# Performance work log

Hardware: AMD Instinct MI355X
Metric: run time of the kernel (lower is better)

Reference implementation:

```python
import jax, jax.numpy as jnp
import numpy as np

D = 256
H = 8
HD = D // H
K = 10
CAP = 500000
B = 256


def setup_inputs() -> dict:
    key = jax.random.key(0)
    ks = jax.random.split(key, 5)
    return {
        "content": jax.random.normal(ks[0], (B, D), dtype=jnp.float32),
        "hologram": jax.random.normal(ks[1], (CAP, D), dtype=jnp.float32),
        "memory_strengths": jnp.ones((CAP,), dtype=jnp.float32),
        "in_proj_w": jax.random.normal(ks[2], (3 * D, D), dtype=jnp.float32) * (1.0 / np.sqrt(D)),
        "in_proj_b": jnp.zeros((3 * D,), dtype=jnp.float32),
        "out_proj_w": jax.random.normal(ks[3], (D, D), dtype=jnp.float32) * (1.0 / np.sqrt(D)),
        "out_proj_b": jnp.zeros((D,), dtype=jnp.float32),
    }


def reference(content, hologram, memory_strengths, in_proj_w, in_proj_b, out_proj_w, out_proj_b):
    # similarities [B, CAP], weighted by per-slot memory strength
    sims = jnp.matmul(content, hologram.T) * memory_strengths[None, :]
    # top-k memory slots per query
    top_vals, top_idx = jax.lax.top_k(sims, K)            # [B, K]
    mem = hologram[top_idx]                               # gather -> [B, K, D]

    # nn.MultiheadAttention (batch_first): packed in-proj split into q/k/v
    wq, wk, wv = in_proj_w[:D], in_proj_w[D:2 * D], in_proj_w[2 * D:]
    bq, bk, bv = in_proj_b[:D], in_proj_b[D:2 * D], in_proj_b[2 * D:]

    q = content @ wq.T + bq                               # [B, D]  (query len 1)
    k = mem @ wk.T + bk                                   # [B, K, D]
    v = mem @ wv.T + bv                                   # [B, K, D]

    qh = q.reshape(B, H, HD)                              # [B, H, HD]
    kh = k.reshape(B, K, H, HD).transpose(0, 2, 1, 3)     # [B, H, K, HD]
    vh = v.reshape(B, K, H, HD).transpose(0, 2, 1, 3)     # [B, H, K, HD]

    scores = jnp.einsum("bhd,bhkd->bhk", qh, kh) / np.sqrt(HD)
    attn = jax.nn.softmax(scores, axis=-1)                # [B, H, K]
    ctx = jnp.einsum("bhk,bhkd->bhd", attn, vh).reshape(B, D)
    recalled = ctx @ out_proj_w.T + out_proj_b            # [B, D]

    # torch MHA returns head-averaged attention weights; query len 1 squeezed
    attn_weights = attn.mean(axis=1)                      # [B, K]
    return recalled, attn_weights
```

## Files before the change

kernel.cpp:

```cpp
#include <hip/hip_runtime.h>
#include <hip/hip_bf16.h>
#include <math.h>

#define D      256
#define H      8
#define HD     32
#define TOPK   10
#define CAP    500000
#define BATCH  256

#define G1     256
#define T1     512
#define NT     32
#define ROUNDS 62
#define CHUNK  (NT*ROUNDS)
#define TOPB   16
#define MSEL   32

typedef float  f32x16 __attribute__((ext_vector_type(16)));
typedef __bf16 bf16x8 __attribute__((ext_vector_type(8)));

union FragCvt { uint4 u; bf16x8 v; };

__device__ __forceinline__ unsigned bfpair(float lo, float hi){
  unsigned a = __builtin_bit_cast(unsigned, lo);
  unsigned b = __builtin_bit_cast(unsigned, hi);
  a += 0x7FFFu + ((a >> 16) & 1u);
  b += 0x7FFFu + ((b >> 16) & 1u);
  return (a >> 16) | (b & 0xFFFF0000u);
}
__device__ __forceinline__ uint4 pack8(float4 p0, float4 p1){
  uint4 u;
  u.x = bfpair(p0.x, p0.y); u.y = bfpair(p0.z, p0.w);
  u.z = bfpair(p1.x, p1.y); u.w = bfpair(p1.z, p1.w);
  return u;
}

__device__ __forceinline__ void list_insert(float (&tv)[TOPB], int (&ti)[TOPB],
                                            float &minv, int &mins, float v, int gi){
  #pragma unroll
  for (int q = 0; q < TOPB; ++q){ if (q == mins){ tv[q] = v; ti[q] = gi; } }
  float mv = tv[0]; int ms = 0;
  #pragma unroll
  for (int q = 1; q < TOPB; ++q){
    float x = tv[q];
    if (x < mv){ mv = x; ms = q; }
  }
  minv = mv; mins = ms;
}

#define ROUND_BODY(R, PAR, I0,I1,I2,I3,IS, S0,S1,S2,S3,SS)                          \
  do {                                                                              \
    {                                              \
      int g  = n0 + ((R)+2)*NT + srow;                                              \
      int gc = (g < CAP) ? g : (CAP-1);                                             \
      int gb = gc*64 + scol*4;                                                      \
      I0 = hf4[gb+0]; I1 = hf4[gb+1]; I2 = hf4[gb+2]; I3 = hf4[gb+3];               \
      if (t < NT){                                                                  \
        int sidx = n0 + ((R)+2)*NT + t;                                             \
        IS = stren[(sidx < CAP) ? sidx : (CAP-1)];                                  \
      }                                                                             \
    }                                                                               \
    f32x16 acc = {0.f,0.f,0.f,0.f,0.f,0.f,0.f,0.f,                                  \
                  0.f,0.f,0.f,0.f,0.f,0.f,0.f,0.f};                                 \
    {          \
      const int bbase = ml*32;                                                      \
      const int kxor  = ml & 7;                                                     \
      _Pragma("unroll")                                                             \
      for (int ks = 0; ks < 16; ++ks){                                              \
        FragCvt fb; fb.u = Bb[PAR][bbase + ((ks*2 + half) ^ kxor)];                 \
        acc = __builtin_amdgcn_mfma_f32_32x32x16_bf16(fb.v, afrag[ks], acc, 0,0,0); \
      }                                                                             \
    }                                                                               \
        \
    if ((R) > 0){                                                                   \
      const int nbasep = n0 + ((R)-1)*NT;                                           \
      const bool fullp = (nbasep + NT) <= CAP;                                      \
      _Pragma("unroll")                                                             \
      for (int j = 0; j < 16; ++j){                                                 \
        const int offj = (j & 3) + 8*(j >> 2) + 4*half;                             \
        bool ok = (svp[j] > minv) && (fullp || (nbasep + offj) < CAP);              \
        if (ok) list_insert(tv, ti, minv, mins, svp[j], nbasep + offj);             \
      }                                                                             \
    }                                                                               \
    {        \
      const float4* s4 = (const float4*)strenb[PAR];                                \
      float4 sg0 = s4[0 + half], sg1 = s4[2 + half],                                \
             sg2 = s4[4 + half], sg3 = s4[6 + half];                                \
      svp[ 0]=acc[ 0]*sg0.x; svp[ 1]=acc[ 1]*sg0.y; svp[ 2]=acc[ 2]*sg0.z;          \
      svp[ 3]=acc[ 3]*sg0.w; svp[ 4]=acc[ 4]*sg1.x; svp[ 5]=acc[ 5]*sg1.y;          \
      svp[ 6]=acc[ 6]*sg1.z; svp[ 7]=acc[ 7]*sg1.w; svp[ 8]=acc[ 8]*sg2.x;          \
      svp[ 9]=acc[ 9]*sg2.y; svp[10]=acc[10]*sg2.z; svp[11]=acc[11]*sg2.w;          \
      svp[12]=acc[12]*sg3.x; svp[13]=acc[13]*sg3.y; svp[14]=acc[14]*sg3.z;          \
      svp[15]=acc[15]*sg3.w;                                                        \
    }                                                                               \
    {                  \
      int kc0 = scol*2;                                                             \
      Bb[(PAR)^1][srow*32 + ((kc0  ) ^ (srow&7))] = pack8(S0, S1);                  \
      Bb[(PAR)^1][srow*32 + ((kc0+1) ^ (srow&7))] = pack8(S2, S3);                  \
      if (t < NT) strenb[(PAR)^1][t] = SS;                                          \
    }                                                                               \
    __syncthreads();                                                                \
  } while (0)

__global__ __launch_bounds__(T1) void k_score(
    const float* __restrict__ content, const float* __restrict__ holo,
    const float* __restrict__ stren, float* __restrict__ cand_val,
    int* __restrict__ cand_idx)
{
  __shared__ uint4 Bb[2][NT*32];
  __shared__ float strenb[2][NT];

  const int t    = threadIdx.x;
  const int lane = t & 63;
  const int w    = t >> 6;
  const int half = lane >> 5;
  const int ml   = lane & 31;

  bf16x8 afrag[16];
  {
    const float4* cf4 = (const float4*)content;
    int base = (w*32 + ml)*64 + half*2;
    #pragma unroll
    for (int ks = 0; ks < 16; ++ks){
      float4 p0 = cf4[base + ks*4 + 0];
      float4 p1 = cf4[base + ks*4 + 1];
      FragCvt fc; fc.u = pack8(p0, p1);
      afrag[ks] = fc.v;
    }
  }

  float tv[TOPB]; int ti[TOPB];
  #pragma unroll
  for (int q = 0; q < TOPB; ++q){ tv[q] = -INFINITY; ti[q] = 0; }
  float minv = -INFINITY; int mins = 0;

  float svp[16];
  #pragma unroll
  for (int j = 0; j < 16; ++j) svp[j] = -INFINITY;

  const int n0 = blockIdx.x * CHUNK;

  const int srow = t >> 4;
  const int scol = t & 15;
  const float4* hf4 = (const float4*)holo;

  float4 a0, a1, a2, a3, b0, b1, b2, b3;
  float  sa = 0.f, sb = 0.f;
  {
    int g  = n0 + srow;
    int gc = (g < CAP) ? g : (CAP-1);
    int gb = gc*64 + scol*4;
    a0 = hf4[gb+0]; a1 = hf4[gb+1]; a2 = hf4[gb+2]; a3 = hf4[gb+3];
    g  = n0 + NT + srow;
    gc = (g < CAP) ? g : (CAP-1);
    gb = gc*64 + scol*4;
    b0 = hf4[gb+0]; b1 = hf4[gb+1]; b2 = hf4[gb+2]; b3 = hf4[gb+3];
    if (t < NT){
      int s0 = n0 + t;
      sa = stren[(s0 < CAP) ? s0 : (CAP-1)];
      int s1 = n0 + NT + t;
      sb = stren[(s1 < CAP) ? s1 : (CAP-1)];
    }
    int kc0 = scol*2;
    Bb[0][srow*32 + ((kc0  ) ^ (srow&7))] = pack8(a0, a1);
    Bb[0][srow*32 + ((kc0+1) ^ (srow&7))] = pack8(a2, a3);
    if (t < NT) strenb[0][t] = sa;
  }
  __syncthreads();

  for (int r = 0; r < ROUNDS; r += 2){
    ROUND_BODY(r,   0, a0,a1,a2,a3,sa,  b0,b1,b2,b3,sb);
    ROUND_BODY(r+1, 1, b0,b1,b2,b3,sb,  a0,a1,a2,a3,sa);
  }
  {
    const int nbasep = n0 + (ROUNDS-1)*NT;
    const bool fullp = (nbasep + NT) <= CAP;
    #pragma unroll
    for (int j = 0; j < 16; ++j){
      const int offj = (j & 3) + 8*(j >> 2) + 4*half;
      bool ok = (svp[j] > minv) && (fullp || (nbasep + offj) < CAP);
      if (ok) list_insert(tv, ti, minv, mins, svp[j], nbasep + offj);
    }
  }

  #pragma unroll
  for (int q = 0; q < TOPB; ++q){
    float ov = __shfl_xor(tv[q], 32);
    int   oi = __shfl_xor(ti[q], 32);
    if (half == 0 && ov > minv) list_insert(tv, ti, minv, mins, ov, oi);
  }
  if (half == 0){
    int m    = w*32 + ml;
    int base = m*(G1*TOPB) + blockIdx.x*TOPB;
    #pragma unroll
    for (int q = 0; q < TOPB; ++q){
      cand_val[base+q] = tv[q];
      cand_idx[base+q] = ti[q];
    }
  }
}

__global__ void k_merge(const float* __restrict__ content,
                        const float* __restrict__ holo,
                        const float* __restrict__ stren,
                        const float* __restrict__ cand_val,
                        const int* __restrict__ cand_idx,
                        int* __restrict__ top_idx)
{
  const int row  = blockIdx.x;
  const int t    = threadIdx.x;
  const int lane = t & 63;
  const int w    = t >> 6;

  float cv[16]; int ci[16];
  {
    int base = row*(G1*TOPB);
    #pragma unroll
    for (int i = 0; i < 16; ++i){
      int c = i*256 + t;
      cv[i] = cand_val[base + c];
      ci[i] = cand_idx[base + c];
    }
  }
  __shared__ float  lv[4];
  __shared__ int    li[4];
  __shared__ int    sel[MSEL];
  __shared__ double ex[MSEL];
  __shared__ float  cont[D];

  for (int s = 0; s < MSEL; ++s){
    float bv = -INFINITY; int bi = 0x7FFFFFFF;
    #pragma unroll
    for (int i = 0; i < 16; ++i){
      if (cv[i] > bv || (cv[i] == bv && ci[i] < bi)){ bv = cv[i]; bi = ci[i]; }
    }
    #pragma unroll
    for (int off = 1; off < 64; off <<= 1){
      float ov = __shfl_xor(bv, off);
      int   oi = __shfl_xor(bi, off);
      if (ov > bv || (ov == bv && oi < bi)){ bv = ov; bi = oi; }
    }
    if (lane == 0){ lv[w] = bv; li[w] = bi; }
    __syncthreads();
    float wv = lv[0]; int wi = li[0];
    #pragma unroll
    for (int q = 1; q < 4; ++q){
      float ov = lv[q]; int oi = li[q];
      if (ov > wv || (ov == wv && oi < wi)){ wv = ov; wi = oi; }
    }
    if (t == 0) sel[s] = wi;
    #pragma unroll
    for (int i = 0; i < 16; ++i){ if (ci[i] == wi) cv[i] = -INFINITY; }
    __syncthreads();
  }
  if (t < 64) ((float4*)cont)[t] = ((const float4*)content)[row*64 + t];
  __syncthreads();

  const float4* hf4 = (const float4*)holo;
  float4 c4 = ((const float4*)cont)[lane];
  for (int q = 0; q < 8; ++q){
    int s   = w*8 + q;
    int idx = sel[s];
    float4 h4 = hf4[idx*64 + lane];
    double a = (double)h4.x*c4.x + (double)h4.y*c4.y + (double)h4.z*c4.z + (double)h4.w*c4.w;
    #pragma unroll
    for (int off = 1; off < 64; off <<= 1) a += __shfl_xor(a, off);
    if (lane == 0) ex[s] = a * (double)stren[idx];
  }
  __syncthreads();
  if (t == 0){
    unsigned used = 0;
    for (int r = 0; r < TOPK; ++r){
      int best = -1;
      for (int c = 0; c < MSEL; ++c){
        if (used & (1u << c)) continue;
        if (best < 0 || ex[c] > ex[best] || (ex[c] == ex[best] && sel[c] < sel[best])) best = c;
      }
      used |= (1u << best);
      top_idx[row*16 + r] = sel[best];
    }
  }
}

__global__ __launch_bounds__(512) void k_attn(
    const float* __restrict__ content, const float* __restrict__ holo,
    const float* __restrict__ inw, const float* __restrict__ inb,
    const float* __restrict__ outw, const float* __restrict__ outb,
    const int* __restrict__ top_idx, float* __restrict__ out)
{
  const int b = blockIdx.x;
  const int t = threadIdx.x;
  __shared__ float cont[D];
  __shared__ float mem_s[TOPK*D];
  __shared__ float q_s[D];
  __shared__ float k_s[TOPK*D];
  __shared__ float v_s[TOPK*D];
  __shared__ float sc[H*TOPK];
  __shared__ float at[H*TOPK];
  __shared__ float ctx[D];

  if (t < 64) ((float4*)cont)[t] = ((const float4*)content)[b*64 + t];
  for (int i = t; i < TOPK*D; i += 512){
    int j = i >> 8; int d = i & 255;
    mem_s[i] = holo[(size_t)top_idx[b*16 + j]*D + d];
  }
  __syncthreads();

  const float4* wf4 = (const float4*)inw;
  if (t < 256){
    float a = 0.f;
    const float4* c4p = (const float4*)cont;
    #pragma unroll 8
    for (int dc = 0; dc < 64; ++dc){
      float4 wv = wf4[t*64 + dc];
      float4 cc = c4p[dc];
      a += wv.x*cc.x + wv.y*cc.y + wv.z*cc.z + wv.w*cc.w;
    }
    q_s[t] = a + inb[t];
  }
  {
    int i    = (t < 256) ? t : (t - 256);
    int wrow = (t < 256) ? (256 + i) : (512 + i);
    float a[10];
    #pragma unroll
    for (int j = 0; j < 10; ++j) a[j] = 0.f;
    const float4* m4 = (const float4*)mem_s;
    for (int dc = 0; dc < 64; ++dc){
      float4 wv = wf4[wrow*64 + dc];
      #pragma unroll
      for (int j = 0; j < 10; ++j){
        float4 mm = m4[j*64 + dc];
        a[j] += wv.x*mm.x + wv.y*mm.y + wv.z*mm.z + wv.w*mm.w;
      }
    }
    float bias = inb[wrow];
    if (t < 256){
      #pragma unroll
      for (int j = 0; j < 10; ++j) k_s[j*256 + i] = a[j] + bias;
    } else {
      #pragma unroll
      for (int j = 0; j < 10; ++j) v_s[j*256 + i] = a[j] + bias;
    }
  }
  __syncthreads();
  if (t < H*TOPK){
    int h = t / TOPK, j = t % TOPK;
    float a = 0.f;
    #pragma unroll
    for (int d = 0; d < HD; ++d) a += q_s[h*HD + d] * k_s[j*256 + h*HD + d];
    sc[t] = a * 0.17677669529663687f;
  }
  __syncthreads();
  if (t < H){
    float m = -INFINITY;
    #pragma unroll
    for (int j = 0; j < 10; ++j) m = fmaxf(m, sc[t*10 + j]);
    float e[10]; float su = 0.f;
    #pragma unroll
    for (int j = 0; j < 10; ++j){ e[j] = expf(sc[t*10 + j] - m); su += e[j]; }
    float inv = 1.f / su;
    #pragma unroll
    for (int j = 0; j < 10; ++j) at[t*10 + j] = e[j]*inv;
  }
  __syncthreads();
  if (t < TOPK){
    float a = 0.f;
    #pragma unroll
    for (int h = 0; h < H; ++h) a += at[h*10 + t];
    out[BATCH*D + b*TOPK + t] = a * 0.125f;
  }
  if (t < 256){
    int h = t >> 5;
    float a = 0.f;
    #pragma unroll
    for (int j = 0; j < 10; ++j) a += at[h*10 + j] * v_s[j*256 + t];
    ctx[t] = a;
  }
  __syncthreads();
  if (t < 256){
    const float4* of4 = (const float4*)outw;
    const float4* c4p = (const float4*)ctx;
    float a = 0.f;
    #pragma unroll 8
    for (int dc = 0; dc < 64; ++dc){
      float4 wv = of4[t*64 + dc];
      float4 cc = c4p[dc];
      a += wv.x*cc.x + wv.y*cc.y + wv.z*cc.z + wv.w*cc.w;
    }
    out[b*D + t] = a + outb[t];
  }
}

extern "C" void kernel_launch(void* const* d_in, const int* in_sizes, int n_in,
                              void* d_out, int out_size, void* d_ws, size_t ws_size,
                              hipStream_t stream) {
  const float* content = (const float*)d_in[0];
  const float* holo    = (const float*)d_in[1];
  const float* stren   = (const float*)d_in[2];
  const float* inw     = (const float*)d_in[3];
  const float* inb     = (const float*)d_in[4];
  const float* outw    = (const float*)d_in[5];
  const float* outb    = (const float*)d_in[6];
  float* out = (float*)d_out;

  float* cand_val = (float*)d_ws;
  int*   cand_idx = (int*)(cand_val + BATCH*G1*TOPB);
  int*   top_idx  = (int*)(cand_idx + BATCH*G1*TOPB);

  hipLaunchKernelGGL(k_score, dim3(G1), dim3(T1), 0, stream,
                     content, holo, stren, cand_val, cand_idx);
  hipLaunchKernelGGL(k_merge, dim3(BATCH), dim3(256), 0, stream,
                     content, holo, stren, cand_val, cand_idx, top_idx);
  hipLaunchKernelGGL(k_attn, dim3(BATCH), dim3(512), 0, stream,
                     content, holo, inw, inb, outw, outb, top_idx, out);
}
```

Baseline: 1.014 ms.

## Use ballot-driven sparse top-k insertion and single-stage register prefetch

Replaces the unrolled per-element conditional insertion into the per-thread top-k list with a bitmask of candidates processed in a wave-uniform loop, so the wave only iterates as many times as the busiest lane needs. It also shortens the global-load prefetch from two rounds ahead to one, halving the staging registers. The aim is to cut divergent insertion cost and register pressure (possibly raising occupancy), at the risk of exposing more global-load latency.

```diff
diff --git a/kernel.cpp b/kernel.cpp
--- a/kernel.cpp
+++ b/kernel.cpp
@@ -49,16 +49,42 @@
   minv = mv; mins = ms;
 }
 
-#define ROUND_BODY(R, PAR, I0,I1,I2,I3,IS, S0,S1,S2,S3,SS)                          \
+__device__ __forceinline__ void select_regs(const float (&sv)[16], int nbase, int half,
+                                            float (&tv)[TOPB], int (&ti)[TOPB],
+                                            float &minv, int &mins){
+  const bool full = (nbase + NT) <= CAP;
+  unsigned pend = 0u;
+  #pragma unroll
+  for (int j = 0; j < 16; ++j){
+    const int offj = (j & 3) + 8*(j >> 2) + 4*half;
+    bool ok = (sv[j] > minv) && (full || (nbase + offj) < CAP);
+    pend |= ok ? (1u << j) : 0u;
+  }
+  while (__any(pend != 0u)){
+    if (pend){
+      int j = __builtin_ctz(pend);
+      pend &= pend - 1u;
+      float v = -INFINITY;
+      #pragma unroll
+      for (int q = 0; q < 16; ++q) v = (q == j) ? sv[q] : v;
+      if (v > minv){
+        int gi = nbase + (j & 3) + 8*(j >> 2) + 4*half;
+        list_insert(tv, ti, minv, mins, v, gi);
+      }
+    }
+  }
+}
+
+#define ROUND_BODY(R, PAR)                                                          \
   do {                                                                              \
     {                                              \
-      int g  = n0 + ((R)+2)*NT + srow;                                              \
+      int g  = n0 + ((R)+1)*NT + srow;                                              \
       int gc = (g < CAP) ? g : (CAP-1);                                             \
       int gb = gc*64 + scol*4;                                                      \
-      I0 = hf4[gb+0]; I1 = hf4[gb+1]; I2 = hf4[gb+2]; I3 = hf4[gb+3];               \
+      a0 = hf4[gb+0]; a1 = hf4[gb+1]; a2 = hf4[gb+2]; a3 = hf4[gb+3];               \
       if (t < NT){                                                                  \
-        int sidx = n0 + ((R)+2)*NT + t;                                             \
-        IS = stren[(sidx < CAP) ? sidx : (CAP-1)];                                  \
+        int sidx = n0 + ((R)+1)*NT + t;                                             \
+        sa = stren[(sidx < CAP) ? sidx : (CAP-1)];                                  \
       }                                                                             \
     }                                                                               \
     f32x16 acc = {0.f,0.f,0.f,0.f,0.f,0.f,0.f,0.f,                                  \
@@ -73,16 +99,7 @@
       }                                                                             \
     }                                                                               \
         \
-    if ((R) > 0){                                                                   \
-      const int nbasep = n0 + ((R)-1)*NT;                                           \
-      const bool fullp = (nbasep + NT) <= CAP;                                      \
-      _Pragma("unroll")                                                             \
-      for (int j = 0; j < 16; ++j){                                                 \
-        const int offj = (j & 3) + 8*(j >> 2) + 4*half;                             \
-        bool ok = (svp[j] > minv) && (fullp || (nbasep + offj) < CAP);              \
-        if (ok) list_insert(tv, ti, minv, mins, svp[j], nbasep + offj);             \
-      }                                                                             \
-    }                                                                               \
+    if ((R) > 0) select_regs(svp, n0 + ((R)-1)*NT, half, tv, ti, minv, mins);       \
     {        \
       const float4* s4 = (const float4*)strenb[PAR];                                \
       float4 sg0 = s4[0 + half], sg1 = s4[2 + half],                                \
@@ -94,11 +111,11 @@
       svp[12]=acc[12]*sg3.x; svp[13]=acc[13]*sg3.y; svp[14]=acc[14]*sg3.z;          \
       svp[15]=acc[15]*sg3.w;                                                        \
     }                                                                               \
-    {                  \
+    {                                         \
       int kc0 = scol*2;                                                             \
-      Bb[(PAR)^1][srow*32 + ((kc0  ) ^ (srow&7))] = pack8(S0, S1);                  \
-      Bb[(PAR)^1][srow*32 + ((kc0+1) ^ (srow&7))] = pack8(S2, S3);                  \
-      if (t < NT) strenb[(PAR)^1][t] = SS;                                          \
+      Bb[(PAR)^1][srow*32 + ((kc0  ) ^ (srow&7))] = pack8(a0, a1);                  \
+      Bb[(PAR)^1][srow*32 + ((kc0+1) ^ (srow&7))] = pack8(a2, a3);                  \
+      if (t < NT) strenb[(PAR)^1][t] = sa;                                          \
     }                                                                               \
     __syncthreads();                                                                \
   } while (0)
@@ -145,22 +162,16 @@
   const int scol = t & 15;
   const float4* hf4 = (const float4*)holo;
 
-  float4 a0, a1, a2, a3, b0, b1, b2, b3;
-  float  sa = 0.f, sb = 0.f;
+  float4 a0, a1, a2, a3;
+  float  sa = 0.f;
   {
     int g  = n0 + srow;
     int gc = (g < CAP) ? g : (CAP-1);
     int gb = gc*64 + scol*4;
     a0 = hf4[gb+0]; a1 = hf4[gb+1]; a2 = hf4[gb+2]; a3 = hf4[gb+3];
-    g  = n0 + NT + srow;
-    gc = (g < CAP) ? g : (CAP-1);
-    gb = gc*64 + scol*4;
-    b0 = hf4[gb+0]; b1 = hf4[gb+1]; b2 = hf4[gb+2]; b3 = hf4[gb+3];
     if (t < NT){
       int s0 = n0 + t;
       sa = stren[(s0 < CAP) ? s0 : (CAP-1)];
-      int s1 = n0 + NT + t;
-      sb = stren[(s1 < CAP) ? s1 : (CAP-1)];
     }
     int kc0 = scol*2;
     Bb[0][srow*32 + ((kc0  ) ^ (srow&7))] = pack8(a0, a1);
@@ -170,19 +181,10 @@
   __syncthreads();
 
   for (int r = 0; r < ROUNDS; r += 2){
-    ROUND_BODY(r,   0, a0,a1,a2,a3,sa,  b0,b1,b2,b3,sb);
-    ROUND_BODY(r+1, 1, b0,b1,b2,b3,sb,  a0,a1,a2,a3,sa);
-  }
-  {
-    const int nbasep = n0 + (ROUNDS-1)*NT;
-    const bool fullp = (nbasep + NT) <= CAP;
-    #pragma unroll
-    for (int j = 0; j < 16; ++j){
-      const int offj = (j & 3) + 8*(j >> 2) + 4*half;
-      bool ok = (svp[j] > minv) && (fullp || (nbasep + offj) < CAP);
-      if (ok) list_insert(tv, ti, minv, mins, svp[j], nbasep + offj);
-    }
-  }
+    ROUND_BODY(r,   0);
+    ROUND_BODY(r+1, 1);
+  }
+  select_regs(svp, n0 + (ROUNDS-1)*NT, half, tv, ti, minv, mins);
 
   #pragma unroll
   for (int q = 0; q < TOPB; ++q){
```

Result: faster. 972.0 us (-4.1%).
